# Kernel optimization log

Measured on AMD Instinct MI355X. Metric: run time of the kernel, lower is better.

The kernel has to match this reference:

```python
import jax, jax.numpy as jnp
import numpy as np

G = 64; B = 4; PER = 25000; N = B * PER
C_SEM = 64; C_MOS = 64; C = 32; NCLS = 26
OFFS = [(dx, dy, dz) for dx in (-1, 0, 1) for dy in (-1, 0, 1) for dz in (-1, 0, 1)]  # 27 kernel offsets


def _build_sparse():
    """Random active voxels per batch + [N,27] submanifold neighbor map (-1 = absent)."""
    rng = np.random.default_rng(0)
    keys_l, coords_l = [], []
    for b in range(B):
        lin = np.sort(rng.choice(G ** 3, size=PER, replace=False))
        x, y, z = lin // (G * G), (lin // G) % G, lin % G
        coords_l.append(np.stack([np.full(PER, b), x, y, z], 1))
        keys_l.append(b * (G ** 3) + lin)
    keys = np.concatenate(keys_l)
    co = np.concatenate(coords_l)
    order = np.argsort(keys, kind='stable')
    sk = keys[order]
    nbr = np.full((N, 27), -1, np.int64)
    bx, x, y, z = co[:, 0], co[:, 1], co[:, 2], co[:, 3]
    for k, (dx, dy, dz) in enumerate(OFFS):
        nx, ny, nz = x + dx, y + dy, z + dz
        ok = (nx >= 0) & (nx < G) & (ny >= 0) & (ny < G) & (nz >= 0) & (nz < G)
        nk = bx * (G ** 3) + nx * (G * G) + ny * G + nz
        pos = np.clip(np.searchsorted(sk, nk), 0, N - 1)
        hit = ok & (sk[pos] == nk)
        nbr[:, k] = np.where(hit, order[pos], -1)
    return co[:, 0].astype(np.int32), nbr.astype(np.int32)


def setup_inputs() -> dict:
    key = jax.random.key(0)
    ks = jax.random.split(key, 16)
    bids, nbr = _build_sparse()
    nrm = lambda k, s: jax.random.normal(ks[k], s, jnp.float32) * 0.05
    return {
        'feat_sem': jax.random.normal(ks[0], (N, C_SEM), jnp.float32),
        'feat_mos': jax.random.normal(ks[1], (N, C_MOS), jnp.float32),
        'fus_sp_w': nrm(2, (C_MOS, 1)), 'fus_sp_b': jnp.zeros((1,), jnp.float32),
        'fus_ch_w': nrm(3, (C_SEM, C_SEM)), 'fus_ch_b': jnp.zeros((C_SEM,), jnp.float32),
        'conv_w': nrm(4, (27, C_SEM, C)), 'conv_b': jnp.zeros((C,), jnp.float32),
        'r1c1_w': nrm(5, (27, C, C)), 'r1g1': jnp.ones((C,), jnp.float32), 'r1b1': jnp.zeros((C,), jnp.float32),
        'r1c2_w': nrm(6, (27, C, C)), 'r1g2': jnp.ones((C,), jnp.float32), 'r1b2': jnp.zeros((C,), jnp.float32),
        'ca1_w': nrm(7, (C, C // 8)), 'ca2_w': nrm(8, (C // 8, C)),
        'r2c1_w': nrm(9, (27, C, C)), 'r2g1': jnp.ones((C,), jnp.float32), 'r2b1': jnp.zeros((C,), jnp.float32),
        'r2c2_w': nrm(10, (27, C, C)), 'r2g2': jnp.ones((C,), jnp.float32), 'r2b2': jnp.zeros((C,), jnp.float32),
        'out_g': jnp.ones((C,), jnp.float32), 'out_b': jnp.zeros((C,), jnp.float32),
        'lin_w': nrm(11, (C, NCLS)), 'lin_b': jnp.zeros((NCLS,), jnp.float32),
        'batch_ids': jnp.asarray(bids), 'nbr': jnp.asarray(nbr), 'num_batches': B,
    }


def _subm3(x, W, nbr, b=None):
    # x: [N,Cin], W: [27,Cin,Cout], nbr: [N,27] (-1 = missing neighbor)
    valid = nbr >= 0
    g = x[jnp.where(valid, nbr, 0)] * valid[..., None].astype(x.dtype)  # [N,27,Cin]
    out = jnp.einsum('nkc,kco->no', g, W)
    return out if b is None else out + b


def _bn(x, g, b, eps=1e-4):
    # BatchNorm1d in training mode: batch stats over N, biased variance
    m = jnp.mean(x, 0)
    v = jnp.mean((x - m) ** 2, 0)
    return (x - m) * jax.lax.rsqrt(v + eps) * g + b


def _seg_mean(x, ids, nb):
    s = jax.ops.segment_sum(x, ids, num_segments=nb)
    c = jax.ops.segment_sum(jnp.ones((x.shape[0], 1), x.dtype), ids, num_segments=nb)
    return s / c


def _forward(feat_sem, feat_mos, fus_sp_w, fus_sp_b, fus_ch_w, fus_ch_b, conv_w, conv_b,
             r1c1_w, r1g1, r1b1, r1c2_w, r1g2, r1b2, ca1_w, ca2_w,
             r2c1_w, r2g1, r2b1, r2c2_w, r2g2, r2b2, out_g, out_b, lin_w, lin_b,
             batch_ids, nbr, num_batches):
    # ---- fusion_module_MGA_3D ----
    fm = jax.nn.sigmoid(feat_mos @ fus_sp_w + fus_sp_b) * feat_sem        # [N,Csem]
    vec = _seg_mean(fm, batch_ids, num_batches) @ fus_ch_w + fus_ch_b    # [B,Csem]
    vec = jax.nn.softmax(vec, axis=1) * vec.shape[1]
    fm = fm * vec[batch_ids]
    feat = fm + feat_sem
    # ---- conv ----
    h = _subm3(feat, conv_w, nbr, conv_b)                                # [N,32]

    def resblock(h, c1w, g1, b1, c2w, g2, b2):
        o = jax.nn.relu(_bn(_subm3(h, c1w, nbr), g1, b1))
        o = _bn(_subm3(o, c2w, nbr), g2, b2)
        return jax.nn.relu(o + h)

    h = resblock(h, r1c1_w, r1g1, r1b1, r1c2_w, r1g2, r1b2)
    # ---- ChannelAttention3D ----
    avg = _seg_mean(h, batch_ids, num_batches)
    mx = jax.ops.segment_max(h, batch_ids, num_segments=num_batches)
    mlp = lambda v: jax.nn.relu(v @ ca1_w) @ ca2_w
    att = jax.nn.sigmoid(mlp(avg) + mlp(mx))                             # [B,32]
    h = h * att[batch_ids]
    h = resblock(h, r2c1_w, r2g1, r2b1, r2c2_w, r2g2, r2b2)
    # ---- output layer ----
    h = jax.nn.relu(_bn(h, out_g, out_b))
    return h @ lin_w + lin_b                                             # [N,NCLS]


def reference(feat_sem, feat_mos, fus_sp_w, fus_sp_b, fus_ch_w, fus_ch_b, conv_w, conv_b,
              r1c1_w, r1g1, r1b1, r1c2_w, r1g2, r1b2, ca1_w, ca2_w,
              r2c1_w, r2g1, r2b1, r2c2_w, r2g2, r2b2, out_g, out_b, lin_w, lin_b,
              batch_ids, nbr, num_batches):
    return _forward(feat_sem, feat_mos, fus_sp_w, fus_sp_b, fus_ch_w, fus_ch_b, conv_w, conv_b,
                    r1c1_w, r1g1, r1b1, r1c2_w, r1g2, r1b2, ca1_w, ca2_w,
                    r2c1_w, r2g1, r2b1, r2c2_w, r2g2, r2b2, out_g, out_b, lin_w, lin_b,
                    batch_ids, nbr, num_batches)
```

## Files before the change

### kernel.cpp

```cpp
#include <hip/hip_runtime.h>
#include <math.h>

#define BMAX 4
typedef __attribute__((ext_vector_type(8))) short s16x8;
typedef __attribute__((ext_vector_type(4))) float f32x4;

__device__ __forceinline__ float sigmoidf_(float x) { return 1.f / (1.f + expf(-x)); }

__device__ __forceinline__ ushort f2b(float f) {
    uint u = __float_as_uint(f);
    u = u + 0x7FFFu + ((u >> 16) & 1u);
    return (ushort)(u >> 16);
}
__device__ __forceinline__ uint pk2(float a, float b) {
    return (uint)f2b(a) | ((uint)f2b(b) << 16);
}

__global__ __launch_bounds__(256)
void k_nbrT(const int* __restrict__ nbr, int* __restrict__ nbrT, int N)
{
    __shared__ int l[64 * 27];
    int tid = threadIdx.x;
    int n0 = blockIdx.x * 64;
    int nrows = min(64, N - n0);
    int tot = nrows * 27;
    for (int t = tid; t < tot; t += 256) l[t] = nbr[(size_t)n0 * 27 + t];
    __syncthreads();
    int lane = tid & 63;
    if (lane < nrows) {
        for (int k = tid >> 6; k < 27; k += 4)
            nbrT[(size_t)k * N + n0 + lane] = l[lane * 27 + k];
    }
}

__global__ __launch_bounds__(256)
void k_fuse_s(const float* __restrict__ mos, const float* __restrict__ spw,
              const float* __restrict__ spb, const int* __restrict__ bids,
              float* __restrict__ s_out, float* __restrict__ pc, int N)
{
    __shared__ float lcnt[BMAX];
    int tid = threadIdx.x;
    if (tid < BMAX) lcnt[tid] = 0.f;
    __syncthreads();
    int n = blockIdx.x * 256 + tid;
    if (n < N) {
        const float* mr = mos + (size_t)n * 64;
        float dot = 0.f;
        #pragma unroll
        for (int c = 0; c < 64; c += 4) {
            float4 m4 = *(const float4*)(mr + c);
            float4 w4 = *(const float4*)(spw + c);
            dot += m4.x * w4.x + m4.y * w4.y + m4.z * w4.z + m4.w * w4.w;
        }
        float s = sigmoidf_(dot + spb[0]);
        s_out[n] = s;
        atomicAdd(&lcnt[bids[n]], 1.f);
    }
    __syncthreads();
    if (tid < BMAX) pc[(size_t)blockIdx.x * 4 + tid] = lcnt[tid];
}

__global__ __launch_bounds__(256)
void k_seg_part(const float* __restrict__ fsem, const float* __restrict__ s_buf,
                const int* __restrict__ bids, float* __restrict__ part, int N)
{
    __shared__ float lseg[BMAX * 64];
    int tid = threadIdx.x;
    lseg[tid] = 0.f;
    __syncthreads();
    int c = tid & 63;
    int slot = blockIdx.x * 4 + (tid >> 6);
    int nslots = gridDim.x * 4;
    int chunk = (N + nslots - 1) / nslots;
    int n0 = slot * chunk;
    int n1 = min(N, n0 + chunk);
    float acc = 0.f; int curb = -1;
    int n = n0;
    for (; n + 4 <= n1; n += 4) {
        int b0 = bids[n], b3 = bids[n + 3];
        float s0 = s_buf[n], s1 = s_buf[n + 1], s2 = s_buf[n + 2], s3 = s_buf[n + 3];
        float f0 = fsem[(size_t)n * 64 + c];
        float f1 = fsem[(size_t)(n + 1) * 64 + c];
        float f2 = fsem[(size_t)(n + 2) * 64 + c];
        float f3 = fsem[(size_t)(n + 3) * 64 + c];
        if (b0 == b3) {
            if (b0 != curb) {
                if (curb >= 0) atomicAdd(&lseg[curb * 64 + c], acc);
                acc = 0.f; curb = b0;
            }
            acc += s0 * f0 + s1 * f1 + s2 * f2 + s3 * f3;
        } else {
            int bb[4] = { b0, bids[n + 1], bids[n + 2], b3 };
            float sv[4] = { s0, s1, s2, s3 };
            float fv[4] = { f0, f1, f2, f3 };
            #pragma unroll
            for (int q = 0; q < 4; ++q) {
                if (bb[q] != curb) {
                    if (curb >= 0) atomicAdd(&lseg[curb * 64 + c], acc);
                    acc = 0.f; curb = bb[q];
                }
                acc += sv[q] * fv[q];
            }
        }
    }
    for (; n < n1; ++n) {
        int b = bids[n];
        if (b != curb) {
            if (curb >= 0) atomicAdd(&lseg[curb * 64 + c], acc);
            acc = 0.f; curb = b;
        }
        acc += s_buf[n] * fsem[(size_t)n * 64 + c];
    }
    if (curb >= 0) atomicAdd(&lseg[curb * 64 + c], acc);
    __syncthreads();
    part[(size_t)blockIdx.x * 256 + tid] = lseg[tid];
}

__global__ __launch_bounds__(1024)
void k_seg_red(const float* __restrict__ part, float* __restrict__ seg, int nblk)
{
    __shared__ float l[1024];
    int tid = threadIdx.x;
    int col = tid & 255, grp = tid >> 8;
    float a = 0.f;
    #pragma unroll 8
    for (int j = grp; j < nblk; j += 4) a += part[(size_t)j * 256 + col];
    l[tid] = a;
    __syncthreads();
    if (tid < 256) seg[tid] = l[tid] + l[256 + tid] + l[512 + tid] + l[768 + tid];
}

__global__ void k_vec(const float* __restrict__ seg, const float* __restrict__ pc, int nbc,
                      const float* __restrict__ chw, const float* __restrict__ chb,
                      float* __restrict__ vec, float* __restrict__ cnt_out)
{
    __shared__ float lred[256];
    __shared__ float lcnt[4];
    int tid = threadIdx.x;
    float a = 0.f;
    for (int j = tid >> 2; j < nbc; j += 64) a += pc[(size_t)j * 4 + (tid & 3)];
    lred[tid] = a;
    __syncthreads();
    if (tid < 4) {
        float s = 0.f;
        #pragma unroll 8
        for (int j = 0; j < 64; ++j) s += lred[j * 4 + tid];
        lcnt[tid] = s;
        cnt_out[tid] = s;
    }
    __syncthreads();
    int b = tid >> 6;
    int c = tid & 63;
    float mean = seg[b * 64 + c] / lcnt[b];
    float v = chb[c];
    #pragma unroll 1
    for (int i = 0; i < 64; ++i) {
        float mi = __shfl(mean, i, 64);
        v += mi * chw[i * 64 + c];
    }
    float m = v;
    #pragma unroll
    for (int off = 32; off; off >>= 1) m = fmaxf(m, __shfl_xor(m, off, 64));
    float e = expf(v - m);
    float ssum = e;
    #pragma unroll
    for (int off = 32; off; off >>= 1) ssum += __shfl_xor(ssum, off, 64);
    vec[b * 64 + c] = e / ssum * 64.f;
}

__global__ __launch_bounds__(256)
void k_gate_cvt(const float* __restrict__ fs, const float* __restrict__ s_buf,
                const float* __restrict__ vec, const int* __restrict__ bids,
                ushort* __restrict__ out, int N)
{
    int gid = blockIdx.x * 256 + threadIdx.x;
    if (gid < 64) out[(size_t)N * 64 + gid] = 0;
    int n = gid >> 3;
    if (n >= N) return;
    int c0 = (gid & 7) * 8;
    float s = s_buf[n];
    const float* vr = vec + bids[n] * 64 + c0;
    const float* fr = fs + (size_t)n * 64 + c0;
    float4 f0 = *(const float4*)fr, f1 = *(const float4*)(fr + 4);
    float4 v0 = *(const float4*)vr, v1 = *(const float4*)(vr + 4);
    float g0 = f0.x * (1.f + s * v0.x), g1 = f0.y * (1.f + s * v0.y);
    float g2 = f0.z * (1.f + s * v0.z), g3 = f0.w * (1.f + s * v0.w);
    float g4 = f1.x * (1.f + s * v1.x), g5 = f1.y * (1.f + s * v1.y);
    float g6 = f1.z * (1.f + s * v1.z), g7 = f1.w * (1.f + s * v1.w);
    uint4 o; o.x = pk2(g0, g1); o.y = pk2(g2, g3); o.z = pk2(g4, g5); o.w = pk2(g6, g7);
    *(uint4*)(out + (size_t)n * 64 + c0) = o;
}

__device__ __forceinline__ void wpack_one(const float* __restrict__ W, int CIN,
                                          int tt, ushort* __restrict__ dst)
{
    int nkc = CIN >> 5;
    int lane = tt & 63;
    int nt = (tt >> 6) & 1;
    int kc = (tt >> 7) % nkc;
    int k = tt / (nkc * 128);
    int kk = kc * 32 + (lane >> 4) * 8;
    int col = nt * 16 + (lane & 15);
    const float* src = W + ((size_t)k * CIN + kk) * 32 + col;
    float v[8];
    #pragma unroll
    for (int e = 0; e < 8; ++e) v[e] = src[e * 32];
    uint4 o; o.x = pk2(v[0], v[1]); o.y = pk2(v[2], v[3]);
    o.z = pk2(v[4], v[5]); o.w = pk2(v[6], v[7]);
    *(uint4*)(dst + (size_t)tt * 8) = o;
}

__global__ __launch_bounds__(256)
void k_wpack_all(const float* __restrict__ W0, const float* __restrict__ W1,
                 const float* __restrict__ W2, const float* __restrict__ W3,
                 const float* __restrict__ W4, ushort* __restrict__ P)
{
    int t = blockIdx.x * 256 + threadIdx.x;
    if (t < 6912) {
        wpack_one(W0, 64, t, P);
    } else {
        int r = t - 6912;
        int s = r / 3456;
        int tt = r % 3456;
        if (s >= 4) return;
        const float* W = (s == 0) ? W1 : (s == 1) ? W2 : (s == 2) ? W3 : W4;
        wpack_one(W, 32, tt, P + 55296 + s * 27648);
    }
}

template<int CIN, bool STATS, bool BIAS, bool WB16>
__global__ __launch_bounds__(256)
void k_mconv(const ushort* __restrict__ inb, const int* __restrict__ nbrT,
             const ushort* __restrict__ wpk, const float* __restrict__ bias,
             float* __restrict__ outf, ushort* __restrict__ outb,
             float* __restrict__ pp, int N)
{
    __shared__ float lsum[32];
    __shared__ float lsq[32];
    int tid = threadIdx.x;
    if (WB16 && blockIdx.x == 0 && tid < 32) outb[(size_t)N * 32 + tid] = 0;
    if (STATS) {
        if (tid < 32) { lsum[tid] = 0.f; lsq[tid] = 0.f; }
        __syncthreads();
    }
    int lane = tid & 63;
    int gw = (blockIdx.x * 256 + tid) >> 6;
    int vbase = gw * 16;
    float ps0 = 0.f, pq0 = 0.f, ps1 = 0.f, pq1 = 0.f;
    if (vbase < N) {
        int row = lane & 15;
        int koff = (lane >> 4) * 8;
        int vr = vbase + row; if (vr >= N) vr = N - 1;
        f32x4 acc0 = {0.f,0.f,0.f,0.f}, acc1 = {0.f,0.f,0.f,0.f};
        int j[27];
        #pragma unroll
        for (int k = 0; k < 27; ++k) j[k] = nbrT[(size_t)k * N + vr];
        #pragma unroll
        for (int k = 0; k < 27; ++k) {
            int jj = (j[k] < 0) ? N : j[k];
            const ushort* arow = inb + (size_t)jj * CIN + koff;
            #pragma unroll
            for (int kc = 0; kc < CIN / 32; ++kc) {
                s16x8 a = *(const s16x8*)(arow + kc * 32);
                const ushort* wb = wpk + (size_t)(k * (CIN / 32) + kc) * 1024 + lane * 8;
                s16x8 b0 = *(const s16x8*)(wb);
                s16x8 b1 = *(const s16x8*)(wb + 512);
                acc0 = __builtin_amdgcn_mfma_f32_16x16x32_bf16(a, b0, acc0, 0, 0, 0);
                acc1 = __builtin_amdgcn_mfma_f32_16x16x32_bf16(a, b1, acc1, 0, 0, 0);
            }
        }
        int ccol = lane & 15;
        int crow = (lane >> 4) * 4;
        float b0v = BIAS ? bias[ccol] : 0.f;
        float b1v = BIAS ? bias[16 + ccol] : 0.f;
        #pragma unroll
        for (int i = 0; i < 4; ++i) {
            int v = vbase + crow + i;
            if (v < N) {
                float x0 = acc0[i] + b0v;
                float x1 = acc1[i] + b1v;
                outf[(size_t)v * 32 + ccol] = x0;
                outf[(size_t)v * 32 + 16 + ccol] = x1;
                if (WB16) {
                    outb[(size_t)v * 32 + ccol] = f2b(x0);
                    outb[(size_t)v * 32 + 16 + ccol] = f2b(x1);
                }
                if (STATS) { ps0 += x0; pq0 += x0 * x0; ps1 += x1; pq1 += x1 * x1; }
            }
        }
    }
    if (STATS) {
        ps0 += __shfl_xor(ps0, 16, 64); ps0 += __shfl_xor(ps0, 32, 64);
        pq0 += __shfl_xor(pq0, 16, 64); pq0 += __shfl_xor(pq0, 32, 64);
        ps1 += __shfl_xor(ps1, 16, 64); ps1 += __shfl_xor(ps1, 32, 64);
        pq1 += __shfl_xor(pq1, 16, 64); pq1 += __shfl_xor(pq1, 32, 64);
        if (lane < 16) {
            atomicAdd(&lsum[lane], ps0);
            atomicAdd(&lsq[lane], pq0);
            atomicAdd(&lsum[16 + lane], ps1);
            atomicAdd(&lsq[16 + lane], pq1);
        }
        __syncthreads();
        if (tid < 32) {
            pp[(size_t)blockIdx.x * 64 + tid] = lsum[tid];
            pp[(size_t)blockIdx.x * 64 + 32 + tid] = lsq[tid];
        }
    }
}

__global__ __launch_bounds__(1024)
void k_statsr(const float* __restrict__ part, int nblk,
              const float* __restrict__ g, const float* __restrict__ bb,
              float* __restrict__ sc, float* __restrict__ sh, float invN)
{
    __shared__ float l[1024];
    int tid = threadIdx.x;
    int col = tid & 63, grp = tid >> 6;
    float a = 0.f;
    #pragma unroll 8
    for (int j = grp; j < nblk; j += 16) a += part[(size_t)j * 64 + col];
    l[tid] = a;
    __syncthreads();
    if (tid < 64) {
        float s = 0.f;
        #pragma unroll
        for (int gq = 0; gq < 16; ++gq) s += l[gq * 64 + tid];
        l[tid] = s;
    }
    __syncthreads();
    if (tid < 32) {
        float m = l[tid] * invN;
        float v = l[32 + tid] * invN - m * m;
        float s = g[tid] * rsqrtf(v + 1e-4f);
        sc[tid] = s;
        sh[tid] = bb[tid] - m * s;
    }
}

__global__ __launch_bounds__(256)
void k_bnact(const float* __restrict__ t, const float* __restrict__ sc,
             const float* __restrict__ sh, ushort* __restrict__ out, int N)
{
    int gid = blockIdx.x * 256 + threadIdx.x;
    if (gid < 32) out[(size_t)N * 32 + gid] = 0;
    int n = gid >> 2;
    if (n >= N) return;
    int c0 = (gid & 3) * 8;
    const float* tr = t + (size_t)n * 32 + c0;
    float4 t0 = *(const float4*)tr, t1 = *(const float4*)(tr + 4);
    float g0 = fmaxf(t0.x * sc[c0+0] + sh[c0+0], 0.f);
    float g1 = fmaxf(t0.y * sc[c0+1] + sh[c0+1], 0.f);
    float g2 = fmaxf(t0.z * sc[c0+2] + sh[c0+2], 0.f);
    float g3 = fmaxf(t0.w * sc[c0+3] + sh[c0+3], 0.f);
    float g4 = fmaxf(t1.x * sc[c0+4] + sh[c0+4], 0.f);
    float g5 = fmaxf(t1.y * sc[c0+5] + sh[c0+5], 0.f);
    float g6 = fmaxf(t1.z * sc[c0+6] + sh[c0+6], 0.f);
    float g7 = fmaxf(t1.w * sc[c0+7] + sh[c0+7], 0.f);
    uint4 o; o.x = pk2(g0, g1); o.y = pk2(g2, g3); o.z = pk2(g4, g5); o.w = pk2(g6, g7);
    *(uint4*)(out + (size_t)n * 32 + c0) = o;
}

__global__ __launch_bounds__(256)
void k_comb1(const float* __restrict__ t, const float* __restrict__ sc,
             const float* __restrict__ sh, const int* __restrict__ bids,
             float* hr, float* __restrict__ part, int N)
{
    __shared__ float lsum[BMAX * 32];
    __shared__ int   lmax[BMAX * 32];
    int tid = threadIdx.x;
    if (tid < BMAX * 32) { lsum[tid] = 0.f; lmax[tid] = 0; }
    __syncthreads();
    int gid = blockIdx.x * 256 + tid;
    int n = gid >> 2;
    int c0 = (gid & 3) * 8;
    if (n < N) {
        int b = bids[n];
        const float* tr = t + (size_t)n * 32 + c0;
        float* rr = hr + (size_t)n * 32 + c0;
        float4 t0 = *(const float4*)tr, t1 = *(const float4*)(tr + 4);
        float4 r0 = *(const float4*)rr, r1 = *(const float4*)(rr + 4);
        float v[8];
        v[0] = fmaxf(t0.x * sc[c0+0] + sh[c0+0] + r0.x, 0.f);
        v[1] = fmaxf(t0.y * sc[c0+1] + sh[c0+1] + r0.y, 0.f);
        v[2] = fmaxf(t0.z * sc[c0+2] + sh[c0+2] + r0.z, 0.f);
        v[3] = fmaxf(t0.w * sc[c0+3] + sh[c0+3] + r0.w, 0.f);
        v[4] = fmaxf(t1.x * sc[c0+4] + sh[c0+4] + r1.x, 0.f);
        v[5] = fmaxf(t1.y * sc[c0+5] + sh[c0+5] + r1.y, 0.f);
        v[6] = fmaxf(t1.z * sc[c0+6] + sh[c0+6] + r1.z, 0.f);
        v[7] = fmaxf(t1.w * sc[c0+7] + sh[c0+7] + r1.w, 0.f);
        float4 o0 = { v[0], v[1], v[2], v[3] };
        float4 o1 = { v[4], v[5], v[6], v[7] };
        *(float4*)rr = o0;
        *(float4*)(rr + 4) = o1;
        int base = b * 32 + c0;
        #pragma unroll
        for (int i = 0; i < 8; ++i) {
            atomicAdd(&lsum[base + i], v[i]);
            atomicMax(&lmax[base + i], __float_as_int(v[i]));
        }
    }
    __syncthreads();
    if (tid < 128) part[(size_t)blockIdx.x * 256 + tid] = lsum[tid];
    else           part[(size_t)blockIdx.x * 256 + tid] = __int_as_float(lmax[tid - 128]);
}

__global__ __launch_bounds__(256)
void k_attred(const float* __restrict__ part, int nblk, float* __restrict__ out)
{
    int tid = threadIdx.x;
    int blk = blockIdx.x;
    if (tid < 128) {
        float a = 0.f;
        #pragma unroll 4
        for (int j = blk; j < nblk; j += 64) a += part[(size_t)j * 256 + tid];
        out[(size_t)blk * 256 + tid] = a;
    } else {
        float m = 0.f;
        #pragma unroll 4
        for (int j = blk; j < nblk; j += 64) m = fmaxf(m, part[(size_t)j * 256 + tid]);
        out[(size_t)blk * 256 + tid] = m;
    }
}

__global__ void k_att(const float* __restrict__ part2, const float* __restrict__ cnt,
                      const float* __restrict__ ca1, const float* __restrict__ ca2,
                      float* __restrict__ att)
{
    __shared__ float seg[256];
    int tid = threadIdx.x;
    if (tid < 128) {
        float a = 0.f;
        #pragma unroll 8
        for (int j = 0; j < 64; ++j) a += part2[j * 256 + tid];
        seg[tid] = a;
    } else {
        float m = 0.f;
        #pragma unroll 8
        for (int j = 0; j < 64; ++j) m = fmaxf(m, part2[j * 256 + tid]);
        seg[tid] = m;
    }
    __syncthreads();
    int b = tid >> 6;
    int lane = tid & 63;
    bool actc = lane < 32;
    int c = lane & 31;
    float avg = actc ? seg[b * 32 + c] / cnt[b] : 0.f;
    float mx  = actc ? seg[128 + b * 32 + c] : 0.f;
    float h[8];
    #pragma unroll
    for (int i = 0; i < 4; ++i) {
        float w = actc ? ca1[c * 4 + i] : 0.f;
        h[i] = avg * w;
        h[i + 4] = mx * w;
    }
    #pragma unroll
    for (int off = 32; off; off >>= 1) {
        #pragma unroll
        for (int i = 0; i < 8; ++i) h[i] += __shfl_xor(h[i], off, 64);
    }
    if (actc) {
        float o = 0.f;
        #pragma unroll
        for (int i = 0; i < 4; ++i)
            o += (fmaxf(h[i], 0.f) + fmaxf(h[i + 4], 0.f)) * ca2[i * 32 + c];
        att[b * 32 + c] = sigmoidf_(o);
    }
}

__global__ __launch_bounds__(256)
void k_scale_cvt(const float* __restrict__ h1, const float* __restrict__ att,
                 const int* __restrict__ bids, float* __restrict__ hatt,
                 ushort* __restrict__ hattb, int N)
{
    int gid = blockIdx.x * 256 + threadIdx.x;
    if (gid < 32) hattb[(size_t)N * 32 + gid] = 0;
    int n = gid >> 2;
    if (n >= N) return;
    int c0 = (gid & 3) * 8;
    const float* hrp = h1 + (size_t)n * 32 + c0;
    const float* ar = att + bids[n] * 32 + c0;
    float4 h0 = *(const float4*)hrp, h1v = *(const float4*)(hrp + 4);
    float4 a0 = *(const float4*)ar, a1 = *(const float4*)(ar + 4);
    float g0 = h0.x * a0.x, g1 = h0.y * a0.y, g2 = h0.z * a0.z, g3 = h0.w * a0.w;
    float g4 = h1v.x * a1.x, g5 = h1v.y * a1.y, g6 = h1v.z * a1.z, g7 = h1v.w * a1.w;
    float4 w0 = { g0, g1, g2, g3 };
    float4 w1 = { g4, g5, g6, g7 };
    *(float4*)(hatt + (size_t)n * 32 + c0) = w0;
    *(float4*)(hatt + (size_t)n * 32 + c0 + 4) = w1;
    uint4 o; o.x = pk2(g0, g1); o.y = pk2(g2, g3); o.z = pk2(g4, g5); o.w = pk2(g6, g7);
    *(uint4*)(hattb + (size_t)n * 32 + c0) = o;
}

__global__ __launch_bounds__(256)
void k_comb2(const float* __restrict__ t, const float* __restrict__ sc,
             const float* __restrict__ sh, float* hr, float* __restrict__ part, int N)
{
    __shared__ float lsum[32];
    __shared__ float lsq[32];
    int tid = threadIdx.x;
    if (tid < 32) { lsum[tid] = 0.f; lsq[tid] = 0.f; }
    __syncthreads();
    int gid = blockIdx.x * 256 + tid;
    int n = gid >> 2;
    int c0 = (gid & 3) * 8;
    if (n < N) {
        const float* tr = t + (size_t)n * 32 + c0;
        float* rr = hr + (size_t)n * 32 + c0;
        float4 t0 = *(const float4*)tr, t1 = *(const float4*)(tr + 4);
        float4 h0 = *(const float4*)rr, h1 = *(const float4*)(rr + 4);
        float v[8];
        v[0] = fmaxf(t0.x * sc[c0+0] + sh[c0+0] + h0.x, 0.f);
        v[1] = fmaxf(t0.y * sc[c0+1] + sh[c0+1] + h0.y, 0.f);
        v[2] = fmaxf(t0.z * sc[c0+2] + sh[c0+2] + h0.z, 0.f);
        v[3] = fmaxf(t0.w * sc[c0+3] + sh[c0+3] + h0.w, 0.f);
        v[4] = fmaxf(t1.x * sc[c0+4] + sh[c0+4] + h1.x, 0.f);
        v[5] = fmaxf(t1.y * sc[c0+5] + sh[c0+5] + h1.y, 0.f);
        v[6] = fmaxf(t1.z * sc[c0+6] + sh[c0+6] + h1.z, 0.f);
        v[7] = fmaxf(t1.w * sc[c0+7] + sh[c0+7] + h1.w, 0.f);
        float4 o0 = { v[0], v[1], v[2], v[3] };
        float4 o1 = { v[4], v[5], v[6], v[7] };
        *(float4*)rr = o0;
        *(float4*)(rr + 4) = o1;
        #pragma unroll
        for (int i = 0; i < 8; ++i) {
            atomicAdd(&lsum[c0 + i], v[i]);
            atomicAdd(&lsq[c0 + i], v[i] * v[i]);
        }
    }
    __syncthreads();
    if (tid < 32) {
        part[(size_t)blockIdx.x * 64 + tid] = lsum[tid];
        part[(size_t)blockIdx.x * 64 + 32 + tid] = lsq[tid];
    }
}

__global__ __launch_bounds__(256)
void k_final(const float* __restrict__ h2, const float* __restrict__ sc,
             const float* __restrict__ sh, const float* __restrict__ lw,
             const float* __restrict__ lb, float* __restrict__ out, int N)
{
    int n = blockIdx.x * 256 + threadIdx.x;
    if (n >= N) return;
    const float* hr = h2 + (size_t)n * 32;
    float acc[26];
    #pragma unroll
    for (int o = 0; o < 26; ++o) acc[o] = lb[o];
    #pragma unroll
    for (int c4 = 0; c4 < 32; c4 += 4) {
        float4 hv = *(const float4*)(hr + c4);
        float xs[4] = { hv.x, hv.y, hv.z, hv.w };
        #pragma unroll
        for (int cc = 0; cc < 4; ++cc) {
            int c = c4 + cc;
            float x = fmaxf(xs[cc] * sc[c] + sh[c], 0.f);
            const float* wr = lw + c * 26;
            #pragma unroll
            for (int o = 0; o < 26; ++o) acc[o] += x * wr[o];
        }
    }
    float* orow = out + (size_t)n * 26;
    #pragma unroll
    for (int o = 0; o < 26; ++o) orow[o] = acc[o];
}

extern "C" void kernel_launch(void* const* d_in, const int* in_sizes, int n_in,
                              void* d_out, int out_size, void* d_ws, size_t ws_size,
                              hipStream_t stream)
{
    const float* feat_sem = (const float*)d_in[0];
    const float* feat_mos = (const float*)d_in[1];
    const float* fus_sp_w = (const float*)d_in[2];
    const float* fus_sp_b = (const float*)d_in[3];
    const float* fus_ch_w = (const float*)d_in[4];
    const float* fus_ch_b = (const float*)d_in[5];
    const float* conv_w   = (const float*)d_in[6];
    const float* conv_b   = (const float*)d_in[7];
    const float* r1c1_w   = (const float*)d_in[8];
    const float* r1g1     = (const float*)d_in[9];
    const float* r1b1     = (const float*)d_in[10];
    const float* r1c2_w   = (const float*)d_in[11];
    const float* r1g2     = (const float*)d_in[12];
    const float* r1b2     = (const float*)d_in[13];
    const float* ca1_w    = (const float*)d_in[14];
    const float* ca2_w    = (const float*)d_in[15];
    const float* r2c1_w   = (const float*)d_in[16];
    const float* r2g1     = (const float*)d_in[17];
    const float* r2b1     = (const float*)d_in[18];
    const float* r2c2_w   = (const float*)d_in[19];
    const float* r2g2     = (const float*)d_in[20];
    const float* r2b2     = (const float*)d_in[21];
    const float* out_g    = (const float*)d_in[22];
    const float* out_b    = (const float*)d_in[23];
    const float* lin_w    = (const float*)d_in[24];
    const float* lin_b    = (const float*)d_in[25];
    const int*   bids     = (const int*)d_in[26];
    const int*   nbr      = (const int*)d_in[27];
    int N = in_sizes[0] / 64;

    float* ws = (float*)d_ws;
    float* S1 = ws;
    float* S2 = ws + (size_t)32 * N;
    float* S3 = ws + (size_t)64 * N;
    ushort* BB1 = (ushort*)(ws + (size_t)96 * N + 32);
    ushort* BB2 = BB1 + (size_t)32 * (N + 16);
    float* sbuf = S2;
    ushort* FGB = (ushort*)S3;
    float* segpart = S1;
    float* st = ws + (size_t)128 * N + 1024;
    float* seg_fm = st;
    float* cnt    = st + 256;
    float* vec    = st + 260;
    float* bnsc   = st + 516;
    float* bnsh   = st + 676;
    float* attbuf = st + 840;
    float* pcnt   = st + 1024;
    float* ppbuf  = st + 4096;
    float* partbuf= ppbuf + ((size_t)(N + 63) / 64) * 64 + 64;
    float* at2    = partbuf + ((size_t)4 * N + 255) / 256 * 256 + 256;
    ushort* wpk0  = (ushort*)(at2 + 16384);
    ushort* wpk1 = wpk0 + 55296;
    ushort* wpk2 = wpk1 + 27648;
    ushort* wpk3 = wpk2 + 27648;
    ushort* wpk4 = wpk3 + 27648;
    int* nbrT = (int*)(wpk0 + 165888);

    int nb  = (N + 255) / 256;
    int nb4 = (4 * N + 255) / 256;
    int nb8 = (8 * N + 255) / 256;
    int nw  = (N + 63) / 64;
    const int NSEG = 512;
    float invN = 1.f / (float)N;

    k_wpack_all<<<81, 256, 0, stream>>>(conv_w, r1c1_w, r1c2_w, r2c1_w, r2c2_w, wpk0);
    k_nbrT<<<nw, 256, 0, stream>>>(nbr, nbrT, N);

    k_fuse_s<<<nb, 256, 0, stream>>>(feat_mos, fus_sp_w, fus_sp_b, bids, sbuf, pcnt, N);
    k_seg_part<<<NSEG, 256, 0, stream>>>(feat_sem, sbuf, bids, segpart, N);
    k_seg_red<<<1, 1024, 0, stream>>>(segpart, seg_fm, NSEG);
    k_vec<<<1, 256, 0, stream>>>(seg_fm, pcnt, nb, fus_ch_w, fus_ch_b, vec, cnt);
    k_gate_cvt<<<nb8, 256, 0, stream>>>(feat_sem, sbuf, vec, bids, FGB, N);

    k_mconv<64, false, true, true><<<nw, 256, 0, stream>>>(FGB, nbrT, wpk0, conv_b,
        S1, BB1, nullptr, N);

    k_mconv<32, true, false, false><<<nw, 256, 0, stream>>>(BB1, nbrT, wpk1, nullptr,
        S2, nullptr, ppbuf, N);
    k_statsr<<<1, 1024, 0, stream>>>(ppbuf, nw, r1g1, r1b1, bnsc + 0, bnsh + 0, invN);
    k_bnact<<<nb4, 256, 0, stream>>>(S2, bnsc + 0, bnsh + 0, BB2, N);

    k_mconv<32, true, false, false><<<nw, 256, 0, stream>>>(BB2, nbrT, wpk2, nullptr,
        S3, nullptr, ppbuf, N);
    k_statsr<<<1, 1024, 0, stream>>>(ppbuf, nw, r1g2, r1b2, bnsc + 32, bnsh + 32, invN);

    k_comb1<<<nb4, 256, 0, stream>>>(S3, bnsc + 32, bnsh + 32, bids, S1, partbuf, N);
    k_attred<<<64, 256, 0, stream>>>(partbuf, nb4, at2);
    k_att<<<1, 256, 0, stream>>>(at2, cnt, ca1_w, ca2_w, attbuf);
    k_scale_cvt<<<nb4, 256, 0, stream>>>(S1, attbuf, bids, S2, BB1, N);

    k_mconv<32, true, false, false><<<nw, 256, 0, stream>>>(BB1, nbrT, wpk3, nullptr,
        S3, nullptr, ppbuf, N);
    k_statsr<<<1, 1024, 0, stream>>>(ppbuf, nw, r2g1, r2b1, bnsc + 64, bnsh + 64, invN);
    k_bnact<<<nb4, 256, 0, stream>>>(S3, bnsc + 64, bnsh + 64, BB2, N);

    k_mconv<32, true, false, false><<<nw, 256, 0, stream>>>(BB2, nbrT, wpk4, nullptr,
        S1, nullptr, ppbuf, N);
    k_statsr<<<1, 1024, 0, stream>>>(ppbuf, nw, r2g2, r2b2, bnsc + 96, bnsh + 96, invN);

    k_comb2<<<nb4, 256, 0, stream>>>(S1, bnsc + 96, bnsh + 96, S2, ppbuf, N);
    k_statsr<<<1, 1024, 0, stream>>>(ppbuf, nb4, out_g, out_b, bnsc + 128, bnsh + 128, invN);

    k_final<<<nb, 256, 0, stream>>>(S2, bnsc + 128, bnsh + 128, lin_w, lin_b, (float*)d_out, N);
}
```

Before: 491.6 us.

## Replace dense 27-offset gather convolution with rulebook pair scatter using atomics

```diff
diff --git a/kernel.cpp b/kernel.cpp
--- a/kernel.cpp
+++ b/kernel.cpp
@@ -2,6 +2,7 @@
 #include <math.h>
 
 #define BMAX 4
+#define CAP 16384
 typedef __attribute__((ext_vector_type(8))) short s16x8;
 typedef __attribute__((ext_vector_type(4))) float f32x4;
 
@@ -17,7 +18,8 @@
 }
 
 __global__ __launch_bounds__(256)
-void k_nbrT(const int* __restrict__ nbr, int* __restrict__ nbrT, int N)
+void k_rule(const int* __restrict__ nbr, int2* __restrict__ pairs,
+            int* __restrict__ gcnt, int N)
 {
     __shared__ int l[64 * 27];
     int tid = threadIdx.x;
@@ -26,10 +28,21 @@
     int tot = nrows * 27;
     for (int t = tid; t < tot; t += 256) l[t] = nbr[(size_t)n0 * 27 + t];
     __syncthreads();
-    int lane = tid & 63;
-    if (lane < nrows) {
-        for (int k = tid >> 6; k < 27; k += 4)
-            nbrT[(size_t)k * N + n0 + lane] = l[lane * 27 + k];
+    int w = tid >> 6, lane = tid & 63;
+    int k0 = w * 7, k1 = min(27, k0 + 7);
+    for (int k = k0; k < k1; ++k) {
+        if (k == 13) continue;
+        int j = (lane < nrows) ? l[lane * 27 + k] : -1;
+        bool valid = j >= 0;
+        unsigned long long mask = __ballot(valid);
+        int cnt = (int)__popcll(mask);
+        int base = 0;
+        if (lane == 0 && cnt) base = atomicAdd(&gcnt[k], cnt);
+        base = __shfl(base, 0, 64);
+        if (valid) {
+            int idx = base + (int)__popcll(mask & ((1ull << lane) - 1ull));
+            if (idx < CAP) pairs[(size_t)k * CAP + idx] = make_int2(j, n0 + lane);
+        }
     }
 }
 
@@ -174,7 +187,6 @@
                 ushort* __restrict__ out, int N)
 {
     int gid = blockIdx.x * 256 + threadIdx.x;
-    if (gid < 64) out[(size_t)N * 64 + gid] = 0;
     int n = gid >> 3;
     if (n >= N) return;
     int c0 = (gid & 7) * 8;
@@ -228,83 +240,111 @@
     }
 }
 
-template<int CIN, bool STATS, bool BIAS, bool WB16>
-__global__ __launch_bounds__(256)
-void k_mconv(const ushort* __restrict__ inb, const int* __restrict__ nbrT,
-             const ushort* __restrict__ wpk, const float* __restrict__ bias,
-             float* __restrict__ outf, ushort* __restrict__ outb,
-             float* __restrict__ pp, int N)
-{
-    __shared__ float lsum[32];
-    __shared__ float lsq[32];
-    int tid = threadIdx.x;
-    if (WB16 && blockIdx.x == 0 && tid < 32) outb[(size_t)N * 32 + tid] = 0;
-    if (STATS) {
-        if (tid < 32) { lsum[tid] = 0.f; lsq[tid] = 0.f; }
-        __syncthreads();
-    }
+template<int CIN, bool BIAS>
+__global__ __launch_bounds__(256)
+void k_center(const ushort* __restrict__ inb, const ushort* __restrict__ wpk13,
+              const float* __restrict__ bias, float* __restrict__ outf, int N)
+{
+    constexpr int NKC = CIN / 32;
+    int tid = threadIdx.x;
     int lane = tid & 63;
     int gw = (blockIdx.x * 256 + tid) >> 6;
     int vbase = gw * 16;
-    float ps0 = 0.f, pq0 = 0.f, ps1 = 0.f, pq1 = 0.f;
-    if (vbase < N) {
-        int row = lane & 15;
-        int koff = (lane >> 4) * 8;
-        int vr = vbase + row; if (vr >= N) vr = N - 1;
-        f32x4 acc0 = {0.f,0.f,0.f,0.f}, acc1 = {0.f,0.f,0.f,0.f};
-        int j[27];
+    if (vbase >= N) return;
+    int row = lane & 15;
+    int koff = (lane >> 4) * 8;
+    int vr = min(vbase + row, N - 1);
+    f32x4 acc0 = {0.f,0.f,0.f,0.f}, acc1 = {0.f,0.f,0.f,0.f};
+    #pragma unroll
+    for (int kc = 0; kc < NKC; ++kc) {
+        s16x8 a = *(const s16x8*)(inb + (size_t)vr * CIN + kc * 32 + koff);
+        const ushort* wb = wpk13 + (size_t)kc * 1024 + lane * 8;
+        s16x8 b0 = *(const s16x8*)(wb);
+        s16x8 b1 = *(const s16x8*)(wb + 512);
+        acc0 = __builtin_amdgcn_mfma_f32_16x16x32_bf16(a, b0, acc0, 0, 0, 0);
+        acc1 = __builtin_amdgcn_mfma_f32_16x16x32_bf16(a, b1, acc1, 0, 0, 0);
+    }
+    int ccol = lane & 15;
+    int crow = (lane >> 4) * 4;
+    float b0v = BIAS ? bias[ccol] : 0.f;
+    float b1v = BIAS ? bias[16 + ccol] : 0.f;
+    #pragma unroll
+    for (int i = 0; i < 4; ++i) {
+        int v = vbase + crow + i;
+        if (v < N) {
+            outf[(size_t)v * 32 + ccol] = acc0[i] + b0v;
+            outf[(size_t)v * 32 + 16 + ccol] = acc1[i] + b1v;
+        }
+    }
+}
+
+template<int CIN>
+__global__ __launch_bounds__(256)
+void k_scatter(const ushort* __restrict__ inb, const int2* __restrict__ pairs,
+               const int* __restrict__ gcnt, const ushort* __restrict__ wpk,
+               float* __restrict__ outf, int N)
+{
+    constexpr int NKC = CIN / 32;
+    int tid = threadIdx.x;
+    int lane = tid & 63;
+    int gw = blockIdx.x * 4 + (tid >> 6);
+    int k = gw >> 10;
+    int tile = gw & 1023;
+    int cnt = min(gcnt[k], CAP);
+    int p0 = tile * 16;
+    if (p0 >= cnt) return;
+    int row = lane & 15;
+    int koff = (lane >> 4) * 8;
+    int pidx = min(p0 + row, cnt - 1);
+    int2 pr = pairs[(size_t)k * CAP + pidx];
+    f32x4 acc0 = {0.f,0.f,0.f,0.f}, acc1 = {0.f,0.f,0.f,0.f};
+    #pragma unroll
+    for (int kc = 0; kc < NKC; ++kc) {
+        s16x8 a = *(const s16x8*)(inb + (size_t)pr.x * CIN + kc * 32 + koff);
+        const ushort* wb = wpk + (size_t)(k * NKC + kc) * 1024 + lane * 8;
+        s16x8 b0 = *(const s16x8*)(wb);
+        s16x8 b1 = *(const s16x8*)(wb + 512);
+        acc0 = __builtin_amdgcn_mfma_f32_16x16x32_bf16(a, b0, acc0, 0, 0, 0);
+        acc1 = __builtin_amdgcn_mfma_f32_16x16x32_bf16(a, b1, acc1, 0, 0, 0);
+    }
+    int ccol = lane & 15;
+    int crow = (lane >> 4) * 4;
+    #pragma unroll
+    for (int i = 0; i < 4; ++i) {
+        int pi = p0 + crow + i;
+        if (pi < cnt) {
+            int outn = pairs[(size_t)k * CAP + pi].y;
+            atomicAdd(&outf[(size_t)outn * 32 + ccol], acc0[i]);
+            atomicAdd(&outf[(size_t)outn * 32 + 16 + ccol], acc1[i]);
+        }
+    }
+}
+
+__global__ __launch_bounds__(256)
+void k_statsp(const float* __restrict__ t, float* __restrict__ part, int N)
+{
+    __shared__ float lsum[32];
+    __shared__ float lsq[32];
+    int tid = threadIdx.x;
+    if (tid < 32) { lsum[tid] = 0.f; lsq[tid] = 0.f; }
+    __syncthreads();
+    int gid = blockIdx.x * 256 + tid;
+    int n = gid >> 2;
+    int c0 = (gid & 3) * 8;
+    if (n < N) {
+        const float* tr = t + (size_t)n * 32 + c0;
+        float4 t0 = *(const float4*)tr, t1 = *(const float4*)(tr + 4);
+        float v[8] = { t0.x, t0.y, t0.z, t0.w, t1.x, t1.y, t1.z, t1.w };
         #pragma unroll
-        for (int k = 0; k < 27; ++k) j[k] = nbrT[(size_t)k * N + vr];
-        #pragma unroll
-        for (int k = 0; k < 27; ++k) {
-            int jj = (j[k] < 0) ? N : j[k];
-            const ushort* arow = inb + (size_t)jj * CIN + koff;
-            #pragma unroll
-            for (int kc = 0; kc < CIN / 32; ++kc) {
-                s16x8 a = *(const s16x8*)(arow + kc * 32);
-                const ushort* wb = wpk + (size_t)(k * (CIN / 32) + kc) * 1024 + lane * 8;
-                s16x8 b0 = *(const s16x8*)(wb);
-                s16x8 b1 = *(const s16x8*)(wb + 512);
-                acc0 = __builtin_amdgcn_mfma_f32_16x16x32_bf16(a, b0, acc0, 0, 0, 0);
-                acc1 = __builtin_amdgcn_mfma_f32_16x16x32_bf16(a, b1, acc1, 0, 0, 0);
-            }
-        }
-        int ccol = lane & 15;
-        int crow = (lane >> 4) * 4;
-        float b0v = BIAS ? bias[ccol] : 0.f;
-        float b1v = BIAS ? bias[16 + ccol] : 0.f;
-        #pragma unroll
-        for (int i = 0; i < 4; ++i) {
-            int v = vbase + crow + i;
-            if (v < N) {
-                float x0 = acc0[i] + b0v;
-                float x1 = acc1[i] + b1v;
-                outf[(size_t)v * 32 + ccol] = x0;
-                outf[(size_t)v * 32 + 16 + ccol] = x1;
-                if (WB16) {
-                    outb[(size_t)v * 32 + ccol] = f2b(x0);
-                    outb[(size_t)v * 32 + 16 + ccol] = f2b(x1);
-                }
-                if (STATS) { ps0 += x0; pq0 += x0 * x0; ps1 += x1; pq1 += x1 * x1; }
-            }
-        }
-    }
-    if (STATS) {
-        ps0 += __shfl_xor(ps0, 16, 64); ps0 += __shfl_xor(ps0, 32, 64);
-        pq0 += __shfl_xor(pq0, 16, 64); pq0 += __shfl_xor(pq0, 32, 64);
-        ps1 += __shfl_xor(ps1, 16, 64); ps1 += __shfl_xor(ps1, 32, 64);
-        pq1 += __shfl_xor(pq1, 16, 64); pq1 += __shfl_xor(pq1, 32, 64);
-        if (lane < 16) {
-            atomicAdd(&lsum[lane], ps0);
-            atomicAdd(&lsq[lane], pq0);
-            atomicAdd(&lsum[16 + lane], ps1);
-            atomicAdd(&lsq[16 + lane], pq1);
-        }
-        __syncthreads();
-        if (tid < 32) {
-            pp[(size_t)blockIdx.x * 64 + tid] = lsum[tid];
-            pp[(size_t)blockIdx.x * 64 + 32 + tid] = lsq[tid];
-        }
+        for (int i = 0; i < 8; ++i) {
+            atomicAdd(&lsum[c0 + i], v[i]);
+            atomicAdd(&lsq[c0 + i], v[i] * v[i]);
+        }
+    }
+    __syncthreads();
+    if (tid < 32) {
+        part[(size_t)blockIdx.x * 64 + tid] = lsum[tid];
+        part[(size_t)blockIdx.x * 64 + 32 + tid] = lsq[tid];
     }
 }
 
@@ -338,11 +378,24 @@
 }
 
 __global__ __launch_bounds__(256)
+void k_cvt(const float* __restrict__ t, ushort* __restrict__ out, int N)
+{
+    int gid = blockIdx.x * 256 + threadIdx.x;
+    int n = gid >> 2;
+    if (n >= N) return;
+    int c0 = (gid & 3) * 8;
+    const float* tr = t + (size_t)n * 32 + c0;
+    float4 t0 = *(const float4*)tr, t1 = *(const float4*)(tr + 4);
+    uint4 o; o.x = pk2(t0.x, t0.y); o.y = pk2(t0.z, t0.w);
+    o.z = pk2(t1.x, t1.y); o.w = pk2(t1.z, t1.w);
+    *(uint4*)(out + (size_t)n * 32 + c0) = o;
+}
+
+__global__ __launch_bounds__(256)
 void k_bnact(const float* __restrict__ t, const float* __restrict__ sc,
              const float* __restrict__ sh, ushort* __restrict__ out, int N)
 {
     int gid = blockIdx.x * 256 + threadIdx.x;
-    if (gid < 32) out[(size_t)N * 32 + gid] = 0;
     int n = gid >> 2;
     if (n >= N) return;
     int c0 = (gid & 3) * 8;
@@ -473,7 +526,6 @@
                  ushort* __restrict__ hattb, int N)
 {
     int gid = blockIdx.x * 256 + threadIdx.x;
-    if (gid < 32) hattb[(size_t)N * 32 + gid] = 0;
     int n = gid >> 2;
     if (n >= N) return;
     int c0 = (gid & 3) * 8;
@@ -613,6 +665,7 @@
     float* bnsc   = st + 516;
     float* bnsh   = st + 676;
     float* attbuf = st + 840;
+    int*   gcnt   = (int*)(st + 980);
     float* pcnt   = st + 1024;
     float* ppbuf  = st + 4096;
     float* partbuf= ppbuf + ((size_t)(N + 63) / 64) * 64 + 64;
@@ -622,17 +675,19 @@
     ushort* wpk2 = wpk1 + 27648;
     ushort* wpk3 = wpk2 + 27648;
     ushort* wpk4 = wpk3 + 27648;
-    int* nbrT = (int*)(wpk0 + 165888);
-
-    int nb  = (N + 255) / 256;
-    int nb4 = (4 * N + 255) / 256;
-    int nb8 = (8 * N + 255) / 256;
-    int nw  = (N + 63) / 64;
+    int2* pairs = (int2*)(wpk0 + 165888);
+
+    int nb   = (N + 255) / 256;
+    int nb4  = (4 * N + 255) / 256;
+    int nb8  = (8 * N + 255) / 256;
+    int nw64 = (N + 63) / 64;
+    const int NSC = 27 * 256;
     const int NSEG = 512;
     float invN = 1.f / (float)N;
 
+    hipMemsetAsync(gcnt, 0, 27 * sizeof(int), stream);
     k_wpack_all<<<81, 256, 0, stream>>>(conv_w, r1c1_w, r1c2_w, r2c1_w, r2c2_w, wpk0);
-    k_nbrT<<<nw, 256, 0, stream>>>(nbr, nbrT, N);
+    k_rule<<<nw64, 256, 0, stream>>>(nbr, pairs, gcnt, N);
 
     k_fuse_s<<<nb, 256, 0, stream>>>(feat_mos, fus_sp_w, fus_sp_b, bids, sbuf, pcnt, N);
     k_seg_part<<<NSEG, 256, 0, stream>>>(feat_sem, sbuf, bids, segpart, N);
@@ -640,31 +695,36 @@
     k_vec<<<1, 256, 0, stream>>>(seg_fm, pcnt, nb, fus_ch_w, fus_ch_b, vec, cnt);
     k_gate_cvt<<<nb8, 256, 0, stream>>>(feat_sem, sbuf, vec, bids, FGB, N);
 
-    k_mconv<64, false, true, true><<<nw, 256, 0, stream>>>(FGB, nbrT, wpk0, conv_b,
-        S1, BB1, nullptr, N);
-
-    k_mconv<32, true, false, false><<<nw, 256, 0, stream>>>(BB1, nbrT, wpk1, nullptr,
-        S2, nullptr, ppbuf, N);
-    k_statsr<<<1, 1024, 0, stream>>>(ppbuf, nw, r1g1, r1b1, bnsc + 0, bnsh + 0, invN);
+    k_center<64, true><<<nb4, 256, 0, stream>>>(FGB, wpk0 + 13 * 2048, conv_b, S1, N);
+    k_scatter<64><<<NSC, 256, 0, stream>>>(FGB, pairs, gcnt, wpk0, S1, N);
+    k_cvt<<<nb4, 256, 0, stream>>>(S1, BB1, N);
+
+    k_center<32, false><<<nb4, 256, 0, stream>>>(BB1, wpk1 + 13 * 1024, nullptr, S2, N);
+    k_scatter<32><<<NSC, 256, 0, stream>>>(BB1, pairs, gcnt, wpk1, S2, N);
+    k_statsp<<<nb4, 256, 0, stream>>>(S2, ppbuf, N);
+    k_statsr<<<1, 1024, 0, stream>>>(ppbuf, nb4, r1g1, r1b1, bnsc + 0, bnsh + 0, invN);
     k_bnact<<<nb4, 256, 0, stream>>>(S2, bnsc + 0, bnsh + 0, BB2, N);
 
-    k_mconv<32, true, false, false><<<nw, 256, 0, stream>>>(BB2, nbrT, wpk2, nullptr,
-        S3, nullptr, ppbuf, N);
-    k_statsr<<<1, 1024, 0, stream>>>(ppbuf, nw, r1g2, r1b2, bnsc + 32, bnsh + 32, invN);
+    k_center<32, false><<<nb4, 256, 0, stream>>>(BB2, wpk2 + 13 * 1024, nullptr, S3, N);
+    k_scatter<32><<<NSC, 256, 0, stream>>>(BB2, pairs, gcnt, wpk2, S3, N);
+    k_statsp<<<nb4, 256, 0, stream>>>(S3, ppbuf, N);
+    k_statsr<<<1, 1024, 0, stream>>>(ppbuf, nb4, r1g2, r1b2, bnsc + 32, bnsh + 32, invN);
 
     k_comb1<<<nb4, 256, 0, stream>>>(S3, bnsc + 32, bnsh + 32, bids, S1, partbuf, N);
     k_attred<<<64, 256, 0, stream>>>(partbuf, nb4, at2);
     k_att<<<1, 256, 0, stream>>>(at2, cnt, ca1_w, ca2_w, attbuf);
     k_scale_cvt<<<nb4, 256, 0, stream>>>(S1, attbuf, bids, S2, BB1, N);
 
-    k_mconv<32, true, false, false><<<nw, 256, 0, stream>>>(BB1, nbrT, wpk3, nullptr,
-        S3, nullptr, ppbuf, N);
-    k_statsr<<<1, 1024, 0, stream>>>(ppbuf, nw, r2g1, r2b1, bnsc + 64, bnsh + 64, invN);
+    k_center<32, false><<<nb4, 256, 0, stream>>>(BB1, wpk3 + 13 * 1024, nullptr, S3, N);
+    k_scatter<32><<<NSC, 256, 0, stream>>>(BB1, pairs, gcnt, wpk3, S3, N);
+    k_statsp<<<nb4, 256, 0, stream>>>(S3, ppbuf, N);
+    k_statsr<<<1, 1024, 0, stream>>>(ppbuf, nb4, r2g1, r2b1, bnsc + 64, bnsh + 64, invN);
     k_bnact<<<nb4, 256, 0, stream>>>(S3, bnsc + 64, bnsh + 64, BB2, N);
 
-    k_mconv<32, true, false, false><<<nw, 256, 0, stream>>>(BB2, nbrT, wpk4, nullptr,
-        S1, nullptr, ppbuf, N);
-    k_statsr<<<1, 1024, 0, stream>>>(ppbuf, nw, r2g2, r2b2, bnsc + 96, bnsh + 96, invN);
+    k_center<32, false><<<nb4, 256, 0, stream>>>(BB2, wpk4 + 13 * 1024, nullptr, S1, N);
+    k_scatter<32><<<NSC, 256, 0, stream>>>(BB2, pairs, gcnt, wpk4, S1, N);
+    k_statsp<<<nb4, 256, 0, stream>>>(S1, ppbuf, N);
+    k_statsr<<<1, 1024, 0, stream>>>(ppbuf, nb4, r2g2, r2b2, bnsc + 96, bnsh + 96, invN);
 
     k_comb2<<<nb4, 256, 0, stream>>>(S1, bnsc + 96, bnsh + 96, S2, ppbuf, N);
     k_statsr<<<1, 1024, 0, stream>>>(ppbuf, nb4, out_g, out_b, bnsc + 128, bnsh + 128, invN);
```

After: 927.6 us. 1.89x slower.
